# Optimization experiments

Hardware: AMD Instinct MI355X
Metric: run time of the kernel (lower is better)

## Reference

```python
import jax, jax.numpy as jnp
import numpy as np

NUM_HEADS = 8
BLOCK = 8      # block_size
HALO = 2       # kernel_size (halo width)


def _rel_to_abs(rel):
    # halo-style relative->absolute conversion
    # rel: [B, G, qh, qw, 2*p-1] -> [B, G, qh, qw, p]
    B, G, qh, qw, dim = rel.shape
    p = (dim + 1) // 2
    gap = p - qw
    flat = rel.reshape(B, G, qh, qw * dim)[:, :, :, qw - 1:-1]
    return flat.reshape(B, G, qh, qw, 2 * (p - 1))[:, :, :, :, gap:p + gap]


def _relative_logits(pos_q, pos_emb_h, pos_emb_w):
    # pos_q: [B, G, qb, qb, kd]; pos_emb_*: [kd, 2*p-1]
    rel_w = _rel_to_abs(jnp.einsum('bghwd,dr->bghwr', pos_q, pos_emb_w))  # [B,G,qb,qb,p] key-width
    q_t = pos_q.transpose(0, 1, 3, 2, 4)
    rel_h = _rel_to_abs(jnp.einsum('bgwhd,dr->bgwhr', q_t, pos_emb_h))
    rel_h = rel_h.transpose(0, 1, 3, 2, 4)  # [B,G,qb,qb,p] key-height
    return rel_h[..., :, None] + rel_w[..., None, :]  # [B,G,qb,qb,p,p]


def reference(x, w_q, w_kv, w_out, pos_emb_h, pos_emb_w):
    B, H, W, C = x.shape
    kd = C // NUM_HEADS                # per-head key dim
    kvk = BLOCK + 2 * HALO             # halo window size
    out_ch = w_out.shape[1]
    v_dim = out_ch // NUM_HEADS
    kv_per_head = (C + out_ch) // NUM_HEADS
    hh, ww = H // BLOCK, W // BLOCK
    scale = float(1.0 / np.sqrt(kd))

    # ---- query (1x1 conv == matmul), blockify ----
    q = (x @ w_q).reshape(B, hh, BLOCK, ww, BLOCK, NUM_HEADS, kd)
    q = q.transpose(0, 5, 1, 3, 2, 4, 6)  # [B,nh,hh,ww,qb,qb,kd]
    attn_q = q.reshape(B, NUM_HEADS, hh, ww, BLOCK * BLOCK, kd) * scale
    pos_q = q.reshape(B, NUM_HEADS * hh * ww, BLOCK, BLOCK, kd)

    # ---- key/value: 1x1 conv, halo pad, unfold into overlapping windows ----
    kv = jnp.pad(x @ w_kv, ((0, 0), (HALO, HALO), (HALO, HALO), (0, 0)))
    idx = np.arange(hh)[:, None] * BLOCK + np.arange(kvk)[None, :]  # [hh,kvk]
    idy = np.arange(ww)[:, None] * BLOCK + np.arange(kvk)[None, :]  # [ww,kvk]
    patches = kv[:, idx][:, :, :, idy]           # [B,hh,kvk,ww,kvk,kv_dim]
    patches = patches.transpose(0, 1, 3, 2, 4, 5)  # [B,hh,ww,kvk,kvk,kv_dim]
    kvh = patches.reshape(B, hh, ww, kvk, kvk, NUM_HEADS, kv_per_head)
    kvh = kvh.transpose(0, 5, 1, 2, 3, 4, 6).reshape(B, NUM_HEADS, hh, ww, kvk * kvk, kv_per_head)
    key, value = kvh[..., :kd], kvh[..., kd:]

    # ---- attention with relative position bias ----
    scores = jnp.einsum('bnhwqd,bnhwkd->bnhwqk', attn_q, key)
    pos = _relative_logits(pos_q, pos_emb_h, pos_emb_w)
    pos = pos.reshape(B, NUM_HEADS, hh, ww, BLOCK * BLOCK, kvk * kvk)
    attn = jax.nn.softmax(scores + pos, axis=-1)
    out = jnp.einsum('bnhwqk,bnhwkv->bnhwqv', attn, value)  # [B,nh,hh,ww,qb*qb,v_dim]

    # ---- de-blockify, output projection ----
    out = out.reshape(B, NUM_HEADS, hh, ww, BLOCK, BLOCK, v_dim)
    out = out.transpose(0, 2, 4, 3, 5, 1, 6).reshape(B, H, W, NUM_HEADS * v_dim)
    return out @ w_out


def setup_inputs() -> dict:
    key = jax.random.key(0)
    ks = jax.random.split(key, 6)
    B, H, W, C = 4, 128, 128, 256
    out_ch = 256
    kd = C // NUM_HEADS
    kvk = BLOCK + 2 * HALO
    std = kd ** -0.5
    return {
        'x': jax.random.normal(ks[0], (B, H, W, C), jnp.float32),
        'w_q': jax.random.normal(ks[1], (C, C), jnp.float32) * 0.02,
        'w_kv': jax.random.normal(ks[2], (C, C + out_ch), jnp.float32) * 0.02,
        'w_out': jax.random.normal(ks[3], (C, out_ch), jnp.float32) * 0.02,
        'pos_emb_h': jax.random.normal(ks[4], (kd, 2 * kvk - 1), jnp.float32) * std,
        'pos_emb_w': jax.random.normal(ks[5], (kd, 2 * kvk - 1), jnp.float32) * std,
    }
```

## Files before the change

### kernel.cpp

```cpp
#include <hip/hip_runtime.h>
#include <hip/hip_bf16.h>
#include <cstdint>


#define KVK 12
#define NKEYS 144
#define VT_S 160
#define PT_S 168
#define LOG2E 1.4426950408889634f

typedef unsigned int u32;
typedef unsigned short u16;
typedef __attribute__((ext_vector_type(8))) __bf16 bf16x8;
typedef __attribute__((ext_vector_type(4))) float f32x4;

__device__ __forceinline__ u16 f2bf(float f) {
    u32 x = __float_as_uint(f);
    return (u16)((x + 0x7fffu + ((x >> 16) & 1u)) >> 16);
}
__device__ __forceinline__ u32 cvtpk(float lo, float hi) {
    u32 d;
    asm("v_cvt_pk_bf16_f32 %0, %1, %2" : "=v"(d) : "v"(lo), "v"(hi));
    return d;
}
__device__ __forceinline__ float max3f(float a, float b, float c) {
    float d;
    asm("v_max3_f32 %0, %1, %2, %3" : "=v"(d) : "v"(a), "v"(b), "v"(c));
    return d;
}
__device__ __forceinline__ float exp2a(float x) {
    float d;
    asm("v_exp_f32 %0, %1" : "=v"(d) : "v"(x));
    return d;
}
__device__ __forceinline__ void gload16(const void* g, void* l) {
    __builtin_amdgcn_global_load_lds(
        (const __attribute__((address_space(1))) void*)g,
        (__attribute__((address_space(3))) void*)l, 16, 0, 0);
}
__device__ __forceinline__ u32 pack2(float lo, float hi) {
    return (u32)f2bf(lo) | ((u32)f2bf(hi) << 16);
}

__global__ __launch_bounds__(256) void conv_prep(const float* __restrict__ x,
                                                 u16* __restrict__ xb,
                                                 const float* __restrict__ wq,
                                                 const float* __restrict__ wkv,
                                                 const float* __restrict__ wout,
                                                 u16* __restrict__ wT,
                                                 u16* __restrict__ woutT,
                                                 const float* __restrict__ emb_h,
                                                 const float* __restrict__ emb_w,
                                                 u16* __restrict__ embT) {
    int blk = blockIdx.x, t = threadIdx.x;
    if (blk < 8192) {
        int i = blk * 256 + t;
        const float4* p = reinterpret_cast<const float4*>(x) + (long)i * 2;
        float4 a = p[0], b = p[1];
        uint4 o;
        o.x = pack2(a.x, a.y); o.y = pack2(a.z, a.w);
        o.z = pack2(b.x, b.y); o.w = pack2(b.z, b.w);
        reinterpret_cast<uint4*>(xb)[i] = o;
        return;
    }
    blk -= 8192;
    if (blk < 256) {
        int idx = blk * 256 + t; int nn = idx >> 8, k = idx & 255;
        wT[idx] = f2bf(wq[(long)k * 256 + nn]);
    } else if (blk < 768) {
        int idx = (blk - 256) * 256 + t; int nn = idx >> 8, k = idx & 255;
        float v = wkv[(long)k * 512 + nn];
        if ((nn & 32) == 0) v *= 0.2550348642f;
        wT[65536 + idx] = f2bf(v);
    } else if (blk < 1024) {
        int idx = (blk - 768) * 256 + t; int nn = idx >> 8, k = idx & 255;
        woutT[idx] = f2bf(wout[(long)k * 256 + nn]);
    } else if (blk == 1024) {
        for (int i = t; i < 1024; i += 256) {
            int p = i >> 5, d = i & 31;
            embT[i] = (p < 23) ? f2bf(emb_h[d * 23 + p]) : 0;
        }
    } else {
        for (int i = t; i < 1024; i += 256) {
            int p = i >> 5, d = i & 31;
            embT[1024 + i] = (p < 23) ? f2bf(emb_w[d * 23 + p]) : 0;
        }
    }
}

__global__ __launch_bounds__(256) void gemm_qkv6(const u16* __restrict__ A,
                                                 const u16* __restrict__ WT,
                                                 u16* __restrict__ Qb,
                                                 u16* __restrict__ KVb) {
    __shared__ u16 As[8192];
    __shared__ u16 Bs[8192];
    const int t = threadIdx.x;
    const int w = t >> 6, lane = t & 63;
    const long m0 = (long)blockIdx.x * 128;
    const long n0 = (long)blockIdx.y * 128;
    const int wr = w >> 1, wc = w & 1;
    const int r = lane & 15, g = lane >> 4;

    f32x4 acc[4][4];
    #pragma unroll
    for (int i = 0; i < 4; ++i)
        #pragma unroll
        for (int j = 0; j < 4; ++j) acc[i][j] = (f32x4){0.f, 0.f, 0.f, 0.f};

    const u16* Ags[4];
    const u16* Bgs[4];
    #pragma unroll
    for (int cq = 0; cq < 4; ++cq) {
        int u = cq * 256 + w * 64 + lane;
        int panel = u >> 9, row = (u >> 2) & 127, col8 = (u & 3) * 8;
        Ags[cq] = A + (m0 + row) * 256 + panel * 32 + col8;
        Bgs[cq] = WT + (n0 + row) * 256 + panel * 32 + col8;
    }

    for (int k0 = 0; k0 < 256; k0 += 64) {
        #pragma unroll
        for (int cq = 0; cq < 4; ++cq) {
            gload16(Ags[cq] + k0, &As[cq * 2048 + w * 512]);
            gload16(Bgs[cq] + k0, &Bs[cq * 2048 + w * 512]);
        }
        __syncthreads();
        #pragma unroll
        for (int kk = 0; kk < 2; ++kk) {
            bf16x8 a[4], b[4];
            #pragma unroll
            for (int i = 0; i < 4; ++i)
                a[i] = *reinterpret_cast<const bf16x8*>(
                    &As[kk * 4096 + (wr * 64 + i * 16 + r) * 32 + g * 8]);
            #pragma unroll
            for (int j = 0; j < 4; ++j)
                b[j] = *reinterpret_cast<const bf16x8*>(
                    &Bs[kk * 4096 + (wc * 64 + j * 16 + r) * 32 + g * 8]);
            #pragma unroll
            for (int i = 0; i < 4; ++i)
                #pragma unroll
                for (int j = 0; j < 4; ++j)
                    acc[i][j] = __builtin_amdgcn_mfma_f32_16x16x32_bf16(b[j], a[i], acc[i][j], 0, 0, 0);
        }
        __syncthreads();
    }

    const bool isQ = (blockIdx.y < 2);
    #pragma unroll
    for (int i = 0; i < 4; ++i) {
        long row = m0 + wr * 64 + i * 16 + r;
        #pragma unroll
        for (int j = 0; j < 4; ++j) {
            long colb = n0 + wc * 64 + j * 16 + g * 4;
            uint2 st;
            st.x = cvtpk(acc[i][j][0], acc[i][j][1]);
            st.y = cvtpk(acc[i][j][2], acc[i][j][3]);
            if (isQ) *reinterpret_cast<uint2*>(Qb + row * 256 + colb) = st;
            else     *reinterpret_cast<uint2*>(KVb + row * 512 + colb - 256) = st;
        }
    }
}

__global__ __launch_bounds__(256) void mfma_gemm(const u16* __restrict__ A,
                                                 const u16* __restrict__ BT,
                                                 float* __restrict__ C, int N) {
    __shared__ u16 As[8192];
    __shared__ u16 Bs[8192];
    const int t = threadIdx.x;
    const int w = t >> 6, lane = t & 63;
    const long m0 = (long)blockIdx.x * 128;
    const long n0 = (long)blockIdx.y * 128;
    const int wr = w >> 1, wc = w & 1;
    const int r = lane & 15, g = lane >> 4;

    f32x4 acc[4][4];
    #pragma unroll
    for (int i = 0; i < 4; ++i)
        #pragma unroll
        for (int j = 0; j < 4; ++j) acc[i][j] = (f32x4){0.f, 0.f, 0.f, 0.f};

    const u16* Ags[4];
    const u16* Bgs[4];
    #pragma unroll
    for (int cq = 0; cq < 4; ++cq) {
        int u = cq * 256 + w * 64 + lane;
        int panel = u >> 9, row = (u >> 2) & 127, col8 = (u & 3) * 8;
        Ags[cq] = A + (m0 + row) * 256 + panel * 32 + col8;
        Bgs[cq] = BT + (n0 + row) * 256 + panel * 32 + col8;
    }

    for (int k0 = 0; k0 < 256; k0 += 64) {
        #pragma unroll
        for (int cq = 0; cq < 4; ++cq) {
            gload16(Ags[cq] + k0, &As[cq * 2048 + w * 512]);
            gload16(Bgs[cq] + k0, &Bs[cq * 2048 + w * 512]);
        }
        __syncthreads();
        #pragma unroll
        for (int kk = 0; kk < 2; ++kk) {
            bf16x8 a[4], b[4];
            #pragma unroll
            for (int i = 0; i < 4; ++i)
                a[i] = *reinterpret_cast<const bf16x8*>(
                    &As[kk * 4096 + (wr * 64 + i * 16 + r) * 32 + g * 8]);
            #pragma unroll
            for (int j = 0; j < 4; ++j)
                b[j] = *reinterpret_cast<const bf16x8*>(
                    &Bs[kk * 4096 + (wc * 64 + j * 16 + r) * 32 + g * 8]);
            #pragma unroll
            for (int i = 0; i < 4; ++i)
                #pragma unroll
                for (int j = 0; j < 4; ++j)
                    acc[i][j] = __builtin_amdgcn_mfma_f32_16x16x32_bf16(b[j], a[i], acc[i][j], 0, 0, 0);
        }
        __syncthreads();
    }

    #pragma unroll
    for (int i = 0; i < 4; ++i) {
        long row = m0 + wr * 64 + i * 16 + r;
        #pragma unroll
        for (int j = 0; j < 4; ++j) {
            long colb = n0 + wc * 64 + j * 16 + g * 4;
            float4 st = make_float4(acc[i][j][0], acc[i][j][1], acc[i][j][2], acc[i][j][3]);
            *reinterpret_cast<float4*>(C + row * N + colb) = st;
        }
    }
}

__global__ __launch_bounds__(256, 5) void attn_mfma(const u16* __restrict__ Qb,
                                                    const u16* __restrict__ KVb,
                                                    const u16* __restrict__ embT,
                                                    u16* __restrict__ Ob) {
    __shared__ __align__(16) char blob[22528];
    u16* Ks  = (u16*)blob;
    u16* Qe  = (u16*)(blob + 18432);
    u16* PT  = (u16*)blob;
    __shared__ u16 Vt[32 * VT_S];

    const int gblk = blockIdx.x;
    const int n = gblk & 7;
    const int bx = (gblk >> 3) & 15;
    const int by = (gblk >> 7) & 15;
    const int b = gblk >> 11;
    const int t = threadIdx.x;
    const int w = t >> 6, lane = t & 63;
    const int g = lane >> 4, r = lane & 15;

    const int q = w * 16 + r;
    const int qi = q >> 3, qj = q & 7;
    const long qrow = ((long)b * 128 + by * 8 + qi) * 128 + bx * 8 + qj;

    bf16x8 qa1 = *reinterpret_cast<const bf16x8*>(Qb + qrow * 256 + n * 32 + g * 8);

    for (int u = t; u < NKEYS * 8; u += 256) {
        int kk = u >> 3, part = u & 7;
        int ky = kk / KVK, kx = kk - ky * KVK;
        int gy = by * 8 + ky - 2, gx = bx * 8 + kx - 2;
        uint4 val = make_uint4(0u, 0u, 0u, 0u);
        if ((unsigned)gy < 128u && (unsigned)gx < 128u) {
            long row = ((long)b * 128 + gy) * 128 + gx;
            val = *reinterpret_cast<const uint4*>(KVb + row * 512 + n * 64 + part * 8);
        }
        if (part < 4) {
            int col = (part * 8) ^ ((kk & 7) << 3);
            *reinterpret_cast<uint4*>(&Ks[kk * 64 + col]) = val;
        } else {
            int d0 = (part - 4) * 8;
            u16 tmp[8];
            *reinterpret_cast<uint4*>(tmp) = val;
            #pragma unroll
            for (int i = 0; i < 8; ++i) {
                int d = d0 + i;
                Vt[d * VT_S + (kk ^ (((d >> 3) & 3) << 3))] = tmp[i];
            }
        }
    }
    for (int u = t; u < 576; u += 256) {
        int kk = u >> 2;
        int col = (32 + (u & 3) * 8) ^ ((kk & 7) << 3);
        *reinterpret_cast<uint4*>(&Ks[kk * 64 + col]) = make_uint4(0u, 0u, 0u, 0u);
    }
    if (t < 64) *reinterpret_cast<uint4*>(&Qe[t * 32 + 24]) = make_uint4(0u, 0u, 0u, 0u);
    if (t >= 224) {
        int d = t - 224;
        int sw = ((d >> 3) & 3) << 3;
        *reinterpret_cast<uint4*>(&Vt[d * VT_S + (144 ^ sw)]) = make_uint4(0u, 0u, 0u, 0u);
        *reinterpret_cast<uint4*>(&Vt[d * VT_S + (152 ^ sw)]) = make_uint4(0u, 0u, 0u, 0u);
    }
    __syncthreads();

    {
        bf16x8 ah0 = *reinterpret_cast<const bf16x8*>(embT + r * 32 + g * 8);
        bf16x8 ah1 = *reinterpret_cast<const bf16x8*>(embT + (16 + r) * 32 + g * 8);
        bf16x8 aw0 = *reinterpret_cast<const bf16x8*>(embT + 1024 + r * 32 + g * 8);
        bf16x8 aw1 = *reinterpret_cast<const bf16x8*>(embT + 1024 + (16 + r) * 32 + g * 8);
        f32x4 z = (f32x4){0.f, 0.f, 0.f, 0.f};
        f32x4 rh0 = __builtin_amdgcn_mfma_f32_16x16x32_bf16(ah0, qa1, z, 0, 0, 0);
        f32x4 rh1 = __builtin_amdgcn_mfma_f32_16x16x32_bf16(ah1, qa1, z, 0, 0, 0);
        f32x4 rw0 = __builtin_amdgcn_mfma_f32_16x16x32_bf16(aw0, qa1, z, 0, 0, 0);
        f32x4 rw1 = __builtin_amdgcn_mfma_f32_16x16x32_bf16(aw1, qa1, z, 0, 0, 0);
        #pragma unroll
        for (int ti = 0; ti < 2; ++ti) {
            #pragma unroll
            for (int e = 0; e < 4; ++e) {
                int p = ti * 16 + g * 4 + e;
                float vh = (ti ? rh1[e] : rh0[e]) * LOG2E;
                float vw = (ti ? rw1[e] : rw0[e]) * LOG2E;
                int kyd = p + qi - 11;
                int kxd = p + qj - 11;
                if ((unsigned)kyd < 12u) Qe[q * 32 + kyd] = f2bf(vh);
                if ((unsigned)kxd < 12u) Qe[q * 32 + 12 + kxd] = f2bf(vw);
            }
        }
        if (t < NKEYS) {
            int ky = (t * 171) >> 11;
            int kx = t - 12 * ky;
            int sw = (t & 7) << 3;
            Ks[t * 64 + ((32 + ky) ^ sw)] = 0x3F80;
            Ks[t * 64 + ((44 + kx) ^ sw)] = 0x3F80;
        }
    }
    __syncthreads();

    bf16x8 qa2 = *reinterpret_cast<const bf16x8*>(&Qe[q * 32 + g * 8]);
    f32x4 acc[9];
    #pragma unroll
    for (int j = 0; j < 9; ++j) {
        int krow = j * 16 + r;
        int sw = (r & 7) << 3;
        bf16x8 kb0 = *reinterpret_cast<const bf16x8*>(&Ks[krow * 64 + ((g * 8) ^ sw)]);
        bf16x8 kb1 = *reinterpret_cast<const bf16x8*>(&Ks[krow * 64 + ((32 + g * 8) ^ sw)]);
        f32x4 z = (f32x4){0.f, 0.f, 0.f, 0.f};
        acc[j] = __builtin_amdgcn_mfma_f32_16x16x32_bf16(kb1, qa2,
                 __builtin_amdgcn_mfma_f32_16x16x32_bf16(kb0, qa1, z, 0, 0, 0), 0, 0, 0);
    }

    float mx = max3f(acc[0][0], acc[0][1], acc[0][2]);
    mx = fmaxf(mx, acc[0][3]);
    #pragma unroll
    for (int j = 1; j < 9; ++j)
        mx = max3f(mx, max3f(acc[j][0], acc[j][1], acc[j][2]), acc[j][3]);
    mx = fmaxf(mx, __shfl_xor(mx, 16));
    mx = fmaxf(mx, __shfl_xor(mx, 32));
    float s0 = 0.f, s1 = 0.f, s2 = 0.f, s3 = 0.f;
    u32 pkA[9], pkB[9];
    #pragma unroll
    for (int j = 0; j < 9; ++j) {
        float e0 = exp2a(acc[j][0] - mx);
        float e1 = exp2a(acc[j][1] - mx);
        float e2 = exp2a(acc[j][2] - mx);
        float e3 = exp2a(acc[j][3] - mx);
        s0 += e0; s1 += e1; s2 += e2; s3 += e3;
        pkA[j] = cvtpk(e0, e1);
        pkB[j] = cvtpk(e2, e3);
    }
    float sum = (s0 + s1) + (s2 + s3);
    sum += __shfl_xor(sum, 16);
    sum += __shfl_xor(sum, 32);
    const float inv = __builtin_amdgcn_rcpf(sum);

    __syncthreads();

    {
        const int ptb = q * PT_S;
        #pragma unroll
        for (int j = 0; j < 9; ++j) {
            *reinterpret_cast<u32*>(&PT[ptb + 16 * j + 4 * g]) = pkA[j];
            *reinterpret_cast<u32*>(&PT[ptb + 16 * j + 4 * g + 2]) = pkB[j];
        }
    }
    if (t < 64) {
        *reinterpret_cast<uint4*>(&PT[t * PT_S + 144]) = make_uint4(0u, 0u, 0u, 0u);
        *reinterpret_cast<uint4*>(&PT[t * PT_S + 152]) = make_uint4(0u, 0u, 0u, 0u);
    }
    __syncthreads();

    const int sw0 = (r >> 3) << 3;
    const int sw1 = (2 + (r >> 3)) << 3;
    f32x4 o0 = (f32x4){0.f, 0.f, 0.f, 0.f};
    f32x4 o1 = (f32x4){0.f, 0.f, 0.f, 0.f};
    #pragma unroll
    for (int kk = 0; kk < 5; ++kk) {
        bf16x8 pb = *reinterpret_cast<const bf16x8*>(&PT[q * PT_S + kk * 32 + g * 8]);
        bf16x8 va0 = *reinterpret_cast<const bf16x8*>(&Vt[r * VT_S + ((kk * 32 + g * 8) ^ sw0)]);
        bf16x8 va1 = *reinterpret_cast<const bf16x8*>(&Vt[(16 + r) * VT_S + ((kk * 32 + g * 8) ^ sw1)]);
        o0 = __builtin_amdgcn_mfma_f32_16x16x32_bf16(va0, pb, o0, 0, 0, 0);
        o1 = __builtin_amdgcn_mfma_f32_16x16x32_bf16(va1, pb, o1, 0, 0, 0);
    }
    {
        uint2 st0, st1;
        st0.x = cvtpk(o0[0] * inv, o0[1] * inv);
        st0.y = cvtpk(o0[2] * inv, o0[3] * inv);
        st1.x = cvtpk(o1[0] * inv, o1[1] * inv);
        st1.y = cvtpk(o1[2] * inv, o1[3] * inv);
        *reinterpret_cast<uint2*>(Ob + qrow * 256 + n * 32 + g * 4) = st0;
        *reinterpret_cast<uint2*>(Ob + qrow * 256 + n * 32 + 16 + g * 4) = st1;
    }
}

extern "C" void kernel_launch(void* const* d_in, const int* in_sizes, int n_in,
                              void* d_out, int out_size, void* d_ws, size_t ws_size,
                              hipStream_t stream) {
    const float* x     = (const float*)d_in[0];
    const float* w_q   = (const float*)d_in[1];
    const float* w_kv  = (const float*)d_in[2];
    const float* w_out = (const float*)d_in[3];
    const float* emb_h = (const float*)d_in[4];
    const float* emb_w = (const float*)d_in[5];

    u16* xb = (u16*)d_out;
    u16* Qb = (u16*)((char*)d_out + (size_t)33554432);
    char* ws = (char*)d_ws;
    u16* KVb   = (u16*)(ws);
    u16* Ob    = (u16*)(ws + (size_t)67108864);
    u16* wT    = (u16*)(ws + (size_t)100663296);
    u16* woutT = (u16*)(ws + (size_t)100663296 + 393216);
    u16* embT  = (u16*)(ws + (size_t)100663296 + 524288);

    dim3 blk(256);
    conv_prep<<<dim3(9218), blk, 0, stream>>>(x, xb, w_q, w_kv, w_out, wT, woutT,
                                              emb_h, emb_w, embT);
    gemm_qkv6<<<dim3(512, 6), blk, 0, stream>>>(xb, wT, Qb, KVb);
    attn_mfma<<<dim3(8192), blk, 0, stream>>>(Qb, KVb, embT, Ob);
    mfma_gemm<<<dim3(512, 2), blk, 0, stream>>>(Ob, woutT, (float*)d_out, 256);
}
```

Baseline: 158.4 us.

## Swizzle GEMM block order for L2 reuse and fold one-hot key writes into zero-fill

Both GEMM kernels now use a 1D grid whose block index is remapped so groups of 8 M-tiles sweep all N-tiles together. This is meant to improve L2 reuse of the A panels across N-tiles. The attention kernel now writes the one-hot relative-position columns of the key tile during the same pass that zero-fills the padding. That removes one __syncthreads and a separate scalar store pass. The risk is extra integer arithmetic per thread, and correctness depends on the combined fill exactly reproducing the earlier layout.

```diff
diff --git a/kernel.cpp b/kernel.cpp
--- a/kernel.cpp
+++ b/kernel.cpp
@@ -10,6 +10,7 @@
 #define LOG2E 1.4426950408889634f
 
 typedef unsigned int u32;
+typedef unsigned long long u64;
 typedef unsigned short u16;
 typedef __attribute__((ext_vector_type(8))) __bf16 bf16x8;
 typedef __attribute__((ext_vector_type(4))) float f32x4;
@@ -95,9 +96,12 @@
     __shared__ u16 As[8192];
     __shared__ u16 Bs[8192];
     const int t = threadIdx.x;
+    const int bid = blockIdx.x;
+    const int mIdx = (bid / 48) * 8 + (bid & 7);
+    const int nt = (bid >> 3) % 6;
     const int w = t >> 6, lane = t & 63;
-    const long m0 = (long)blockIdx.x * 128;
-    const long n0 = (long)blockIdx.y * 128;
+    const long m0 = (long)mIdx * 128;
+    const long n0 = (long)nt * 128;
     const int wr = w >> 1, wc = w & 1;
     const int r = lane & 15, g = lane >> 4;
 
@@ -144,7 +148,7 @@
         __syncthreads();
     }
 
-    const bool isQ = (blockIdx.y < 2);
+    const bool isQ = (nt < 2);
     #pragma unroll
     for (int i = 0; i < 4; ++i) {
         long row = m0 + wr * 64 + i * 16 + r;
@@ -166,9 +170,12 @@
     __shared__ u16 As[8192];
     __shared__ u16 Bs[8192];
     const int t = threadIdx.x;
+    const int bid = blockIdx.x;
+    const int mIdx = (bid / 16) * 8 + (bid & 7);
+    const int nt = (bid >> 3) & 1;
     const int w = t >> 6, lane = t & 63;
-    const long m0 = (long)blockIdx.x * 128;
-    const long n0 = (long)blockIdx.y * 128;
+    const long m0 = (long)mIdx * 128;
+    const long n0 = (long)nt * 128;
     const int wr = w >> 1, wc = w & 1;
     const int r = lane & 15, g = lane >> 4;
 
@@ -276,9 +283,20 @@
         }
     }
     for (int u = t; u < 576; u += 256) {
-        int kk = u >> 2;
-        int col = (32 + (u & 3) * 8) ^ ((kk & 7) << 3);
-        *reinterpret_cast<uint4*>(&Ks[kk * 64 + col]) = make_uint4(0u, 0u, 0u, 0u);
+        int kk = u >> 2, uu = u & 3;
+        int ky = (kk * 171) >> 11;
+        int kx = kk - 12 * ky;
+        int hy = ky - 8 * uu;
+        int hx = 12 + kx - 8 * uu;
+        u64 lo = 0, hi = 0;
+        if ((unsigned)hy < 4u) lo |= 0x3F80ULL << (hy * 16);
+        else if ((unsigned)hy < 8u) hi |= 0x3F80ULL << ((hy - 4) * 16);
+        if ((unsigned)hx < 4u) lo |= 0x3F80ULL << (hx * 16);
+        else if ((unsigned)hx < 8u) hi |= 0x3F80ULL << ((hx - 4) * 16);
+        int col = (32 + uu * 8) ^ ((kk & 7) << 3);
+        u64* dst = reinterpret_cast<u64*>(&Ks[kk * 64 + col]);
+        dst[0] = lo;
+        dst[1] = hi;
     }
     if (t < 64) *reinterpret_cast<uint4*>(&Qe[t * 32 + 24]) = make_uint4(0u, 0u, 0u, 0u);
     if (t >= 224) {
@@ -287,7 +305,6 @@
         *reinterpret_cast<uint4*>(&Vt[d * VT_S + (144 ^ sw)]) = make_uint4(0u, 0u, 0u, 0u);
         *reinterpret_cast<uint4*>(&Vt[d * VT_S + (152 ^ sw)]) = make_uint4(0u, 0u, 0u, 0u);
     }
-    __syncthreads();
 
     {
         bf16x8 ah0 = *reinterpret_cast<const bf16x8*>(embT + r * 32 + g * 8);
@@ -312,13 +329,6 @@
                 if ((unsigned)kxd < 12u) Qe[q * 32 + 12 + kxd] = f2bf(vw);
             }
         }
-        if (t < NKEYS) {
-            int ky = (t * 171) >> 11;
-            int kx = t - 12 * ky;
-            int sw = (t & 7) << 3;
-            Ks[t * 64 + ((32 + ky) ^ sw)] = 0x3F80;
-            Ks[t * 64 + ((44 + kx) ^ sw)] = 0x3F80;
-        }
     }
     __syncthreads();
 
@@ -420,7 +430,7 @@
     dim3 blk(256);
     conv_prep<<<dim3(9218), blk, 0, stream>>>(x, xb, w_q, w_kv, w_out, wT, woutT,
                                               emb_h, emb_w, embT);
-    gemm_qkv6<<<dim3(512, 6), blk, 0, stream>>>(xb, wT, Qb, KVb);
+    gemm_qkv6<<<dim3(3072), blk, 0, stream>>>(xb, wT, Qb, KVb);
     attn_mfma<<<dim3(8192), blk, 0, stream>>>(Qb, KVb, embT, Ob);
-    mfma_gemm<<<dim3(512, 2), blk, 0, stream>>>(Ob, woutT, (float*)d_out, 256);
-}
+    mfma_gemm<<<dim3(1024), blk, 0, stream>>>(Ob, woutT, (float*)d_out, 256);
+}
```

New measurement: 146.5 us. 7.5% less time.
